# Kernel optimization log

Hardware: AMD Instinct MI355X
Metric: run time of the kernel (lower is better)

The kernel has to match this reference:

```python
import jax, jax.numpy as jnp
import numpy as np

D_MODEL = 512
N_HEADS = 8
HEAD_DIM = 64
INNER = N_HEADS * HEAD_DIM
PAD = 128  # flash-attention style tile padding used by the custom kernel


def setup_inputs() -> dict:
    key = jax.random.key(0)
    ks = jax.random.split(key, 5)
    B, S = 2, 2048
    scale = 0.02
    return {
        "hidden_states": jax.random.normal(ks[0], (B, S, D_MODEL), dtype=jnp.float32),
        "Wq": jax.random.normal(ks[1], (D_MODEL, INNER), dtype=jnp.float32) * scale,
        "Wk": jax.random.normal(ks[2], (D_MODEL, INNER), dtype=jnp.float32) * scale,
        "Wv": jax.random.normal(ks[3], (D_MODEL, INNER), dtype=jnp.float32) * scale,
        "Wo": jax.random.normal(ks[4], (INNER, D_MODEL), dtype=jnp.float32) * scale,
    }


def _padded_attention(q, k, v):
    """Emulates torch.ops.knl.fwd: pad seq to a multiple of PAD, run
    non-causal scaled dot-product attention masking padded keys, then
    slice back to the original length. q,k,v: [B, S, INNER]."""
    B, S, _ = q.shape
    pad_len = (-S) % PAD
    Sp = S + pad_len
    pad_cfg = ((0, 0), (0, pad_len), (0, 0))
    qp = jnp.pad(q, pad_cfg)
    kp = jnp.pad(k, pad_cfg)
    vp = jnp.pad(v, pad_cfg)
    # [B, H, Sp, hd]
    qh = qp.reshape(B, Sp, N_HEADS, HEAD_DIM).transpose(0, 2, 1, 3)
    kh = kp.reshape(B, Sp, N_HEADS, HEAD_DIM).transpose(0, 2, 1, 3)
    vh = vp.reshape(B, Sp, N_HEADS, HEAD_DIM).transpose(0, 2, 1, 3)
    scale = 1.0 / np.sqrt(HEAD_DIM).astype(np.float32)
    scores = jnp.einsum("bhqd,bhkd->bhqk", qh, kh) * scale  # [B,H,Sp,Sp]
    key_valid = jnp.arange(Sp) < S  # mask out padded keys
    scores = jnp.where(key_valid[None, None, None, :], scores, jnp.float32(-1e30))
    probs = jax.nn.softmax(scores, axis=-1)
    out = jnp.einsum("bhqk,bhkd->bhqd", probs, vh)  # [B,H,Sp,hd]
    out = out.transpose(0, 2, 1, 3).reshape(B, Sp, INNER)
    return out[:, :S, :]


def reference(hidden_states, Wq, Wk, Wv, Wo):
    q = hidden_states @ Wq
    k = hidden_states @ Wk
    v = hidden_states @ Wv
    attn = _padded_attention(q, k, v)
    return attn @ Wo
```

## Files before the change

### kernel.cpp

```cpp
#include <hip/hip_runtime.h>

using bf16 = __bf16;
using bf16x4 = __attribute__((ext_vector_type(4))) __bf16;
using bf16x8 = __attribute__((ext_vector_type(8))) __bf16;
using floatx4 = __attribute__((ext_vector_type(4))) float;
using half4 = __attribute__((ext_vector_type(4))) _Float16;
using half8 = __attribute__((ext_vector_type(8))) _Float16;

#define D_MODEL 512
#define S_LEN 2048
#define HD 64
#define NH 8
#define M_TOT 4096
#define RS 72
#define NSPLIT 4
#define KSPAN (S_LEN / NSPLIT)
#define QSCALE 0.18033688f

__device__ __forceinline__ bf16x8 ld8(const bf16* p) {
    return *reinterpret_cast<const bf16x8*>(p);
}
__device__ __forceinline__ void gl_lds16(const bf16* g, bf16* l) {
    __builtin_amdgcn_global_load_lds(
        (const __attribute__((address_space(1))) void*)g,
        (__attribute__((address_space(3))) void*)l, 16, 0, 0);
}

__global__ __launch_bounds__(256) void prep(const float* __restrict__ w0,
                                            const float* __restrict__ w1,
                                            const float* __restrict__ w2,
                                            const float* __restrict__ w3,
                                            const float* __restrict__ X,
                                            bf16* __restrict__ WT,
                                            bf16* __restrict__ Xb) {
    int z = blockIdx.z;
    if (z == 4) {
        int i = (blockIdx.x * 256 + threadIdx.x) * 8;
        float4 a = *reinterpret_cast<const float4*>(X + i);
        float4 b = *reinterpret_cast<const float4*>(X + i + 4);
        bf16x8 o;
        o[0] = (bf16)a.x; o[1] = (bf16)a.y; o[2] = (bf16)a.z; o[3] = (bf16)a.w;
        o[4] = (bf16)b.x; o[5] = (bf16)b.y; o[6] = (bf16)b.z; o[7] = (bf16)b.w;
        *reinterpret_cast<bf16x8*>(Xb + i) = o;
        return;
    }
    if (blockIdx.x >= 256) return;
    __shared__ float t[32][33];
    const float* in = z == 0 ? w0 : z == 1 ? w1 : z == 2 ? w2 : w3;
    bf16* o = WT + (size_t)z * D_MODEL * D_MODEL;
    int x = threadIdx.x & 31;
    int y = threadIdx.x >> 5;
    int k0 = (blockIdx.x & 15) * 32, n0 = (blockIdx.x >> 4) * 32;
    for (int r = y; r < 32; r += 8) t[r][x] = in[(size_t)(k0 + r) * D_MODEL + n0 + x];
    __syncthreads();
    for (int r = y; r < 32; r += 8) o[(size_t)(n0 + r) * D_MODEL + k0 + x] = (bf16)t[x][r];
}

__global__ __launch_bounds__(256) void transpose_v(const bf16* __restrict__ v,
                                                   bf16* __restrict__ vt) {
    __shared__ bf16 t[32][34];
    int bh = blockIdx.z;
    int s0 = blockIdx.x * 32, d0 = blockIdx.y * 32;
    const bf16* in = v + (size_t)bh * S_LEN * HD;
    bf16* o = vt + (size_t)bh * HD * S_LEN;
    int x = threadIdx.x & 31;
    int y = threadIdx.x >> 5;
    for (int r = y; r < 32; r += 8) t[r][x] = in[(size_t)(s0 + r) * HD + d0 + x];
    __syncthreads();
    for (int r = y; r < 32; r += 8) o[(size_t)(d0 + r) * S_LEN + s0 + x] = t[x][r];
}

__global__ __launch_bounds__(256) void gemm_qkv(const bf16* __restrict__ X,
                                                const bf16* __restrict__ WT3,
                                                bf16* __restrict__ qkv) {
    __shared__ __align__(16) bf16 As[64 * 64];
    __shared__ __align__(16) bf16 Bs[64 * 64];
    int lane = threadIdx.x & 63, wave = threadIdx.x >> 6;
    int l15 = lane & 15, quad = lane >> 4;
    const bf16* wt = WT3 + (size_t)blockIdx.z * D_MODEL * D_MODEL;
    bf16* dst = qkv + (size_t)blockIdx.z * M_TOT * D_MODEL;
    int m0 = blockIdx.x * 64;
    int n0 = blockIdx.y * 64;
    int wm = (wave & 1) * 32, wn = (wave >> 1) * 32;
    float oscale = (blockIdx.z == 0) ? QSCALE : 1.0f;

    int sr = lane >> 3;
    int sc = (lane & 7) ^ sr;
    const bf16* gA = X  + (size_t)(m0 + wave * 16 + sr) * D_MODEL + sc * 8;
    const bf16* gB = wt + (size_t)(n0 + wave * 16 + sr) * D_MODEL + sc * 8;
    bf16* ldsA = &As[(wave * 16) * 64];
    bf16* ldsB = &Bs[(wave * 16) * 64];
    int rx = l15 & 7;

    floatx4 acc[2][2] = {};
    for (int k0 = 0; k0 < D_MODEL; k0 += 64) {
        __syncthreads();
        gl_lds16(gA + k0, ldsA);
        gl_lds16(gA + (size_t)8 * D_MODEL + k0, ldsA + 8 * 64);
        gl_lds16(gB + k0, ldsB);
        gl_lds16(gB + (size_t)8 * D_MODEL + k0, ldsB + 8 * 64);
        __syncthreads();
        bf16x8 af[2][2], bfr[2][2];
        #pragma unroll
        for (int mt = 0; mt < 2; mt++)
            #pragma unroll
            for (int kh = 0; kh < 2; kh++)
                af[mt][kh] = ld8(&As[(wm + mt * 16 + l15) * 64 + (((quad + 4 * kh) ^ rx)) * 8]);
        #pragma unroll
        for (int nt = 0; nt < 2; nt++)
            #pragma unroll
            for (int kh = 0; kh < 2; kh++)
                bfr[nt][kh] = ld8(&Bs[(wn + nt * 16 + l15) * 64 + (((quad + 4 * kh) ^ rx)) * 8]);
        #pragma unroll
        for (int mt = 0; mt < 2; mt++)
            #pragma unroll
            for (int nt = 0; nt < 2; nt++) {
                acc[mt][nt] = __builtin_amdgcn_mfma_f32_16x16x32_bf16(af[mt][0], bfr[nt][0], acc[mt][nt], 0, 0, 0);
                acc[mt][nt] = __builtin_amdgcn_mfma_f32_16x16x32_bf16(af[mt][1], bfr[nt][1], acc[mt][nt], 0, 0, 0);
            }
    }

    #pragma unroll
    for (int mt = 0; mt < 2; mt++)
        #pragma unroll
        for (int nt = 0; nt < 2; nt++)
            #pragma unroll
            for (int r = 0; r < 4; r++) {
                int m = m0 + wm + mt * 16 + quad * 4 + r;
                int n = n0 + wn + nt * 16 + l15;
                int b = m >> 11, s = m & 2047;
                int h = n >> 6,  d = n & 63;
                dst[((size_t)(b * NH + h) * S_LEN + s) * HD + d] = (bf16)(acc[mt][nt][r] * oscale);
            }
}

__global__ __launch_bounds__(256) void attn_split(const bf16* __restrict__ qg,
                                                  const bf16* __restrict__ kg,
                                                  const bf16* __restrict__ vt,
                                                  _Float16* __restrict__ Opart,
                                                  float* __restrict__ lsum) {
    __shared__ __align__(16) bf16 Kl[64 * 64];
    __shared__ __align__(16) bf16 Vl[64 * 64];
    __shared__ __align__(16) bf16 Pl[128 * RS];
    int tid = threadIdx.x;
    int lane = tid & 63, wave = tid >> 6;
    int l15 = lane & 15, quad = lane >> 4;
    int bh = blockIdx.y, split = blockIdx.z;
    int q0 = blockIdx.x * 128;
    const bf16* qb = qg + (size_t)bh * S_LEN * HD;
    const bf16* kb = kg + (size_t)bh * S_LEN * HD + (size_t)split * KSPAN * HD;
    const bf16* vb = vt + (size_t)bh * HD * S_LEN + split * KSPAN;

    int qA = q0 + wave * 32 + l15;
    int qB = qA + 16;
    bf16x8 qf[2][2];
    qf[0][0] = ld8(qb + (size_t)qA * HD + quad * 8);
    qf[0][1] = ld8(qb + (size_t)qA * HD + 32 + quad * 8);
    qf[1][0] = ld8(qb + (size_t)qB * HD + quad * 8);
    qf[1][1] = ld8(qb + (size_t)qB * HD + 32 + quad * 8);
    floatx4 O[2][4] = {};
    float l_i[2] = {0.f, 0.f};

    int sr = lane >> 3;
    int sc = (lane & 7) ^ sr;
    const bf16* gK = kb + (size_t)(wave * 16 + sr) * HD + sc * 8;
    const bf16* gV = vb + (size_t)(wave * 16 + sr) * S_LEN + sc * 8;
    bf16* ldsK = &Kl[(wave * 16) * 64];
    bf16* ldsV = &Vl[(wave * 16) * 64];
    int rx = l15 & 7;

    for (int kt = 0; kt < KSPAN; kt += 64) {
        __syncthreads();
        gl_lds16(gK + (size_t)kt * HD, ldsK);
        gl_lds16(gK + (size_t)(kt + 8) * HD, ldsK + 8 * 64);
        gl_lds16(gV + kt, ldsV);
        gl_lds16(gV + (size_t)8 * S_LEN + kt, ldsV + 8 * 64);
        __syncthreads();

        #pragma unroll
        for (int qh = 0; qh < 2; qh++) {
            floatx4 sc4[4];
            #pragma unroll
            for (int nt = 0; nt < 4; nt++) {
                floatx4 z = {};
                bf16x8 a0 = ld8(&Kl[(nt * 16 + l15) * 64 + (quad ^ rx) * 8]);
                bf16x8 a1 = ld8(&Kl[(nt * 16 + l15) * 64 + ((quad + 4) ^ rx) * 8]);
                z = __builtin_amdgcn_mfma_f32_16x16x32_bf16(a0, qf[qh][0], z, 0, 0, 0);
                z = __builtin_amdgcn_mfma_f32_16x16x32_bf16(a1, qf[qh][1], z, 0, 0, 0);
                sc4[nt] = z;
            }
            #pragma unroll
            for (int nt = 0; nt < 4; nt++) {
                bf16x4 pk;
                #pragma unroll
                for (int r = 0; r < 4; r++) {
                    float p = exp2f(sc4[nt][r]);
                    l_i[qh] += p;
                    pk[r] = (bf16)p;
                }
                *reinterpret_cast<bf16x4*>(
                    &Pl[(wave * 32 + qh * 16 + l15) * RS + nt * 16 + quad * 4]) = pk;
            }
        }
        __syncthreads();

        bf16x8 pb[2][2];
        #pragma unroll
        for (int qh = 0; qh < 2; qh++) {
            pb[qh][0] = ld8(&Pl[(wave * 32 + qh * 16 + l15) * RS + quad * 8]);
            pb[qh][1] = ld8(&Pl[(wave * 32 + qh * 16 + l15) * RS + 32 + quad * 8]);
        }
        #pragma unroll
        for (int nt = 0; nt < 4; nt++) {
            bf16x8 v0 = ld8(&Vl[(nt * 16 + l15) * 64 + (quad ^ rx) * 8]);
            bf16x8 v1 = ld8(&Vl[(nt * 16 + l15) * 64 + ((quad + 4) ^ rx) * 8]);
            #pragma unroll
            for (int qh = 0; qh < 2; qh++) {
                O[qh][nt] = __builtin_amdgcn_mfma_f32_16x16x32_bf16(v0, pb[qh][0], O[qh][nt], 0, 0, 0);
                O[qh][nt] = __builtin_amdgcn_mfma_f32_16x16x32_bf16(v1, pb[qh][1], O[qh][nt], 0, 0, 0);
            }
        }
    }

    #pragma unroll
    for (int qh = 0; qh < 2; qh++) {
        float l = l_i[qh];
        l += __shfl_xor(l, 16, 64);
        l += __shfl_xor(l, 32, 64);
        int q = (qh == 0) ? qA : qB;
        size_t obase = (((size_t)(split * 16 + bh)) * S_LEN + q) * HD;
        #pragma unroll
        for (int nt = 0; nt < 4; nt++) {
            half4 h;
            h[0] = (_Float16)O[qh][nt][0]; h[1] = (_Float16)O[qh][nt][1];
            h[2] = (_Float16)O[qh][nt][2]; h[3] = (_Float16)O[qh][nt][3];
            *reinterpret_cast<half4*>(&Opart[obase + nt * 16 + quad * 4]) = h;
        }
        if (quad == 0)
            lsum[((size_t)(split * 16 + bh)) * S_LEN + q] = l;
    }
}

__global__ __launch_bounds__(256) void attn_merge(const _Float16* __restrict__ Opart,
                                                  const float* __restrict__ lsum,
                                                  bf16* __restrict__ ctx) {
    int idx = blockIdx.x * 256 + threadIdx.x;
    int g = idx & 7;
    int q = (idx >> 3) & 2047;
    int bh = idx >> 14;
    int b = bh >> 3, h = bh & 7;
    float l = 0.f;
    #pragma unroll
    for (int s = 0; s < NSPLIT; s++) l += lsum[((size_t)(s * 16 + bh)) * S_LEN + q];
    float inv = 1.f / l;
    float o[8] = {};
    #pragma unroll
    for (int s = 0; s < NSPLIT; s++) {
        half8 hp = *reinterpret_cast<const half8*>(
            &Opart[(((size_t)(s * 16 + bh)) * S_LEN + q) * HD + g * 8]);
        #pragma unroll
        for (int j = 0; j < 8; j++) o[j] += (float)hp[j];
    }
    bf16x8 ob;
    #pragma unroll
    for (int j = 0; j < 8; j++) ob[j] = (bf16)(o[j] * inv);
    *reinterpret_cast<bf16x8*>(&ctx[((size_t)(b * S_LEN + q)) * D_MODEL + h * HD + g * 8]) = ob;
}

__global__ __launch_bounds__(256) void gemm_out(const bf16* __restrict__ Xc,
                                                const bf16* __restrict__ WoT,
                                                float* __restrict__ out) {
    __shared__ __align__(16) bf16 As[64 * 64];
    __shared__ __align__(16) bf16 Bs[64 * 64];
    int lane = threadIdx.x & 63, wave = threadIdx.x >> 6;
    int l15 = lane & 15, quad = lane >> 4;
    int m0 = blockIdx.x * 64;
    int n0 = blockIdx.y * 64;
    int wm = (wave & 1) * 32, wn = (wave >> 1) * 32;

    int sr = lane >> 3;
    int sc = (lane & 7) ^ sr;
    const bf16* gA = Xc  + (size_t)(m0 + wave * 16 + sr) * D_MODEL + sc * 8;
    const bf16* gB = WoT + (size_t)(n0 + wave * 16 + sr) * D_MODEL + sc * 8;
    bf16* ldsA = &As[(wave * 16) * 64];
    bf16* ldsB = &Bs[(wave * 16) * 64];
    int rx = l15 & 7;

    floatx4 acc[2][2] = {};
    for (int k0 = 0; k0 < D_MODEL; k0 += 64) {
        __syncthreads();
        gl_lds16(gA + k0, ldsA);
        gl_lds16(gA + (size_t)8 * D_MODEL + k0, ldsA + 8 * 64);
        gl_lds16(gB + k0, ldsB);
        gl_lds16(gB + (size_t)8 * D_MODEL + k0, ldsB + 8 * 64);
        __syncthreads();
        bf16x8 af[2][2], bfr[2][2];
        #pragma unroll
        for (int mt = 0; mt < 2; mt++)
            #pragma unroll
            for (int kh = 0; kh < 2; kh++)
                af[mt][kh] = ld8(&As[(wm + mt * 16 + l15) * 64 + (((quad + 4 * kh) ^ rx)) * 8]);
        #pragma unroll
        for (int nt = 0; nt < 2; nt++)
            #pragma unroll
            for (int kh = 0; kh < 2; kh++)
                bfr[nt][kh] = ld8(&Bs[(wn + nt * 16 + l15) * 64 + (((quad + 4 * kh) ^ rx)) * 8]);
        #pragma unroll
        for (int mt = 0; mt < 2; mt++)
            #pragma unroll
            for (int nt = 0; nt < 2; nt++) {
                acc[mt][nt] = __builtin_amdgcn_mfma_f32_16x16x32_bf16(af[mt][0], bfr[nt][0], acc[mt][nt], 0, 0, 0);
                acc[mt][nt] = __builtin_amdgcn_mfma_f32_16x16x32_bf16(af[mt][1], bfr[nt][1], acc[mt][nt], 0, 0, 0);
            }
    }

    #pragma unroll
    for (int mt = 0; mt < 2; mt++)
        #pragma unroll
        for (int nt = 0; nt < 2; nt++)
            #pragma unroll
            for (int r = 0; r < 4; r++) {
                int m = m0 + wm + mt * 16 + quad * 4 + r;
                int n = n0 + wn + nt * 16 + l15;
                out[(size_t)m * D_MODEL + n] = acc[mt][nt][r];
            }
}

extern "C" void kernel_launch(void* const* d_in, const int* in_sizes, int n_in,
                              void* d_out, int out_size, void* d_ws, size_t ws_size,
                              hipStream_t stream) {
    const float* X  = (const float*)d_in[0];
    const float* Wq = (const float*)d_in[1];
    const float* Wk = (const float*)d_in[2];
    const float* Wv = (const float*)d_in[3];
    const float* Wo = (const float*)d_in[4];
    float* out = (float*)d_out;
    bf16* ws  = (bf16*)d_ws;

    bf16* Xb  = ws;
    bf16* WT  = Xb + (size_t)M_TOT * D_MODEL;
    bf16* qkv = WT + (size_t)4 * D_MODEL * D_MODEL;
    bf16* ctx = qkv + (size_t)3 * M_TOT * D_MODEL;
    _Float16* Opart = (_Float16*)(ctx + (size_t)M_TOT * D_MODEL);
    float* lbuf = (float*)(Opart + (size_t)NSPLIT * 16 * S_LEN * HD);
    bf16* VT = Xb;

    prep<<<dim3(1024, 1, 5), 256, 0, stream>>>(Wq, Wk, Wv, Wo, X, WT, Xb);
    gemm_qkv<<<dim3(64, 8, 3), 256, 0, stream>>>(Xb, WT, qkv);
    transpose_v<<<dim3(64, 2, 16), 256, 0, stream>>>(qkv + (size_t)2 * M_TOT * D_MODEL, VT);
    attn_split<<<dim3(16, 16, NSPLIT), 256, 0, stream>>>(qkv,
                                                         qkv + (size_t)M_TOT * D_MODEL,
                                                         VT, Opart, lbuf);
    attn_merge<<<dim3(16 * S_LEN * 8 / 256), 256, 0, stream>>>(Opart, lbuf, ctx);
    gemm_out<<<dim3(64, 8), 256, 0, stream>>>(ctx, WT + (size_t)3 * D_MODEL * D_MODEL, out);
}
```

Baseline: 131.3 us.

## Fuse V transpose into QKV GEMM epilogue and split-merge into output GEMM

The QKV projection now runs as one flattened grid over the concatenated weights. Its epilogue writes V directly in transposed [bh, d, s] layout with packed 4-element stores, which removes the separate transpose_v kernel. The attention split-merge is folded into the output projection: each block sums the per-split partial outputs and normalisers while staging the A tile into LDS, so the attn_merge kernel and the ctx buffer round-trip go away. In exchange, the output GEMM recomputes the merge for every N-block (8x redundant Opart reads), and the A tile now goes through synchronous register loads instead of async global_load_lds.

New measurement: 132.7 us. No clear change (+1.0%).

```diff
diff --git a/kernel.cpp b/kernel.cpp
--- a/kernel.cpp
+++ b/kernel.cpp
@@ -56,38 +56,25 @@
     for (int r = y; r < 32; r += 8) o[(size_t)(n0 + r) * D_MODEL + k0 + x] = (bf16)t[x][r];
 }
 
-__global__ __launch_bounds__(256) void transpose_v(const bf16* __restrict__ v,
-                                                   bf16* __restrict__ vt) {
-    __shared__ bf16 t[32][34];
-    int bh = blockIdx.z;
-    int s0 = blockIdx.x * 32, d0 = blockIdx.y * 32;
-    const bf16* in = v + (size_t)bh * S_LEN * HD;
-    bf16* o = vt + (size_t)bh * HD * S_LEN;
-    int x = threadIdx.x & 31;
-    int y = threadIdx.x >> 5;
-    for (int r = y; r < 32; r += 8) t[r][x] = in[(size_t)(s0 + r) * HD + d0 + x];
-    __syncthreads();
-    for (int r = y; r < 32; r += 8) o[(size_t)(d0 + r) * S_LEN + s0 + x] = t[x][r];
-}
-
-__global__ __launch_bounds__(256) void gemm_qkv(const bf16* __restrict__ X,
-                                                const bf16* __restrict__ WT3,
-                                                bf16* __restrict__ qkv) {
+__global__ __launch_bounds__(256) void gemm_qkvf(const bf16* __restrict__ X,
+                                                 const bf16* __restrict__ WT,
+                                                 bf16* __restrict__ qk,
+                                                 bf16* __restrict__ VT) {
     __shared__ __align__(16) bf16 As[64 * 64];
     __shared__ __align__(16) bf16 Bs[64 * 64];
     int lane = threadIdx.x & 63, wave = threadIdx.x >> 6;
     int l15 = lane & 15, quad = lane >> 4;
-    const bf16* wt = WT3 + (size_t)blockIdx.z * D_MODEL * D_MODEL;
-    bf16* dst = qkv + (size_t)blockIdx.z * M_TOT * D_MODEL;
     int m0 = blockIdx.x * 64;
     int n0 = blockIdx.y * 64;
+    int z = n0 >> 9;
+    int h = (n0 >> 6) & 7;
     int wm = (wave & 1) * 32, wn = (wave >> 1) * 32;
-    float oscale = (blockIdx.z == 0) ? QSCALE : 1.0f;
+    float oscale = (z == 0) ? QSCALE : 1.0f;
 
     int sr = lane >> 3;
     int sc = (lane & 7) ^ sr;
     const bf16* gA = X  + (size_t)(m0 + wave * 16 + sr) * D_MODEL + sc * 8;
-    const bf16* gB = wt + (size_t)(n0 + wave * 16 + sr) * D_MODEL + sc * 8;
+    const bf16* gB = WT + (size_t)(n0 + wave * 16 + sr) * D_MODEL + sc * 8;
     bf16* ldsA = &As[(wave * 16) * 64];
     bf16* ldsB = &Bs[(wave * 16) * 64];
     int rx = l15 & 7;
@@ -120,18 +107,33 @@
             }
     }
 
-    #pragma unroll
-    for (int mt = 0; mt < 2; mt++)
-        #pragma unroll
-        for (int nt = 0; nt < 2; nt++)
-            #pragma unroll
-            for (int r = 0; r < 4; r++) {
-                int m = m0 + wm + mt * 16 + quad * 4 + r;
-                int n = n0 + wn + nt * 16 + l15;
+    if (z < 2) {
+        bf16* dst = qk + (size_t)z * M_TOT * HD * NH;
+        #pragma unroll
+        for (int mt = 0; mt < 2; mt++)
+            #pragma unroll
+            for (int nt = 0; nt < 2; nt++)
+                #pragma unroll
+                for (int r = 0; r < 4; r++) {
+                    int m = m0 + wm + mt * 16 + quad * 4 + r;
+                    int n = wn + nt * 16 + l15;
+                    int b = m >> 11, s = m & 2047;
+                    dst[((size_t)(b * NH + h) * S_LEN + s) * HD + n] = (bf16)(acc[mt][nt][r] * oscale);
+                }
+    } else {
+        #pragma unroll
+        for (int mt = 0; mt < 2; mt++)
+            #pragma unroll
+            for (int nt = 0; nt < 2; nt++) {
+                int m = m0 + wm + mt * 16 + quad * 4;
+                int d = wn + nt * 16 + l15;
                 int b = m >> 11, s = m & 2047;
-                int h = n >> 6,  d = n & 63;
-                dst[((size_t)(b * NH + h) * S_LEN + s) * HD + d] = (bf16)(acc[mt][nt][r] * oscale);
-            }
+                bf16x4 pk;
+                pk[0] = (bf16)acc[mt][nt][0]; pk[1] = (bf16)acc[mt][nt][1];
+                pk[2] = (bf16)acc[mt][nt][2]; pk[3] = (bf16)acc[mt][nt][3];
+                *reinterpret_cast<bf16x4*>(&VT[((size_t)(b * NH + h) * HD + d) * S_LEN + s]) = pk;
+            }
+    }
 }
 
 __global__ __launch_bounds__(256) void attn_split(const bf16* __restrict__ qg,
@@ -241,46 +243,33 @@
     }
 }
 
-__global__ __launch_bounds__(256) void attn_merge(const _Float16* __restrict__ Opart,
-                                                  const float* __restrict__ lsum,
-                                                  bf16* __restrict__ ctx) {
-    int idx = blockIdx.x * 256 + threadIdx.x;
-    int g = idx & 7;
-    int q = (idx >> 3) & 2047;
-    int bh = idx >> 14;
-    int b = bh >> 3, h = bh & 7;
-    float l = 0.f;
-    #pragma unroll
-    for (int s = 0; s < NSPLIT; s++) l += lsum[((size_t)(s * 16 + bh)) * S_LEN + q];
-    float inv = 1.f / l;
-    float o[8] = {};
-    #pragma unroll
-    for (int s = 0; s < NSPLIT; s++) {
-        half8 hp = *reinterpret_cast<const half8*>(
-            &Opart[(((size_t)(s * 16 + bh)) * S_LEN + q) * HD + g * 8]);
-        #pragma unroll
-        for (int j = 0; j < 8; j++) o[j] += (float)hp[j];
-    }
-    bf16x8 ob;
-    #pragma unroll
-    for (int j = 0; j < 8; j++) ob[j] = (bf16)(o[j] * inv);
-    *reinterpret_cast<bf16x8*>(&ctx[((size_t)(b * S_LEN + q)) * D_MODEL + h * HD + g * 8]) = ob;
-}
-
-__global__ __launch_bounds__(256) void gemm_out(const bf16* __restrict__ Xc,
-                                                const bf16* __restrict__ WoT,
-                                                float* __restrict__ out) {
+__global__ __launch_bounds__(256) void gemm_outm(const _Float16* __restrict__ Opart,
+                                                 const float* __restrict__ lsum,
+                                                 const bf16* __restrict__ WoT,
+                                                 float* __restrict__ out) {
     __shared__ __align__(16) bf16 As[64 * 64];
     __shared__ __align__(16) bf16 Bs[64 * 64];
-    int lane = threadIdx.x & 63, wave = threadIdx.x >> 6;
+    __shared__ float invl[64 * 8];
+    int tid = threadIdx.x;
+    int lane = tid & 63, wave = tid >> 6;
     int l15 = lane & 15, quad = lane >> 4;
     int m0 = blockIdx.x * 64;
     int n0 = blockIdx.y * 64;
     int wm = (wave & 1) * 32, wn = (wave >> 1) * 32;
 
+    for (int i = tid; i < 512; i += 256) {
+        int row = i >> 3, h = i & 7;
+        int mm = m0 + row;
+        int b = mm >> 11, q = mm & 2047;
+        float l = 0.f;
+        #pragma unroll
+        for (int s = 0; s < NSPLIT; s++)
+            l += lsum[((size_t)(s * 16 + b * NH + h)) * S_LEN + q];
+        invl[i] = 1.f / l;
+    }
+
     int sr = lane >> 3;
     int sc = (lane & 7) ^ sr;
-    const bf16* gA = Xc  + (size_t)(m0 + wave * 16 + sr) * D_MODEL + sc * 8;
     const bf16* gB = WoT + (size_t)(n0 + wave * 16 + sr) * D_MODEL + sc * 8;
     bf16* ldsA = &As[(wave * 16) * 64];
     bf16* ldsB = &Bs[(wave * 16) * 64];
@@ -289,10 +278,28 @@
     floatx4 acc[2][2] = {};
     for (int k0 = 0; k0 < D_MODEL; k0 += 64) {
         __syncthreads();
-        gl_lds16(gA + k0, ldsA);
-        gl_lds16(gA + (size_t)8 * D_MODEL + k0, ldsA + 8 * 64);
         gl_lds16(gB + k0, ldsB);
         gl_lds16(gB + (size_t)8 * D_MODEL + k0, ldsB + 8 * 64);
+        int h = k0 >> 6;
+        #pragma unroll
+        for (int st = 0; st < 2; st++) {
+            int row = wave * 16 + sr + st * 8;
+            int mm = m0 + row;
+            int b = mm >> 11, q = mm & 2047;
+            float iv = invl[row * 8 + h];
+            float a8[8] = {};
+            #pragma unroll
+            for (int s = 0; s < NSPLIT; s++) {
+                half8 hp = *reinterpret_cast<const half8*>(
+                    &Opart[(((size_t)(s * 16 + b * NH + h)) * S_LEN + q) * HD + sc * 8]);
+                #pragma unroll
+                for (int j = 0; j < 8; j++) a8[j] += (float)hp[j];
+            }
+            bf16x8 v;
+            #pragma unroll
+            for (int j = 0; j < 8; j++) v[j] = (bf16)(a8[j] * iv);
+            *reinterpret_cast<bf16x8*>(ldsA + st * 512 + lane * 8) = v;
+        }
         __syncthreads();
         bf16x8 af[2][2], bfr[2][2];
         #pragma unroll
@@ -339,18 +346,16 @@
 
     bf16* Xb  = ws;
     bf16* WT  = Xb + (size_t)M_TOT * D_MODEL;
-    bf16* qkv = WT + (size_t)4 * D_MODEL * D_MODEL;
-    bf16* ctx = qkv + (size_t)3 * M_TOT * D_MODEL;
-    _Float16* Opart = (_Float16*)(ctx + (size_t)M_TOT * D_MODEL);
+    bf16* qk  = WT + (size_t)4 * D_MODEL * D_MODEL;
+    bf16* VT  = qk + (size_t)2 * M_TOT * D_MODEL;
+    _Float16* Opart = (_Float16*)(VT + (size_t)M_TOT * D_MODEL);
     float* lbuf = (float*)(Opart + (size_t)NSPLIT * 16 * S_LEN * HD);
-    bf16* VT = Xb;
 
     prep<<<dim3(1024, 1, 5), 256, 0, stream>>>(Wq, Wk, Wv, Wo, X, WT, Xb);
-    gemm_qkv<<<dim3(64, 8, 3), 256, 0, stream>>>(Xb, WT, qkv);
-    transpose_v<<<dim3(64, 2, 16), 256, 0, stream>>>(qkv + (size_t)2 * M_TOT * D_MODEL, VT);
-    attn_split<<<dim3(16, 16, NSPLIT), 256, 0, stream>>>(qkv,
-                                                         qkv + (size_t)M_TOT * D_MODEL,
+    gemm_qkvf<<<dim3(64, 24), 256, 0, stream>>>(Xb, WT, qk, VT);
+    attn_split<<<dim3(16, 16, NSPLIT), 256, 0, stream>>>(qk,
+                                                         qk + (size_t)M_TOT * D_MODEL,
                                                          VT, Opart, lbuf);
-    attn_merge<<<dim3(16 * S_LEN * 8 / 256), 256, 0, stream>>>(Opart, lbuf, ctx);
-    gemm_out<<<dim3(64, 8), 256, 0, stream>>>(ctx, WT + (size_t)3 * D_MODEL * D_MODEL, out);
-}
+    gemm_outm<<<dim3(64, 8), 256, 0, stream>>>(Opart, lbuf,
+                                               WT + (size_t)3 * D_MODEL * D_MODEL, out);
+}
```
